# Kernel tuning notes

Hardware: AMD Instinct MI355X
Metric: run time of the kernel (lower is better)

## Reference

```python
import jax, jax.numpy as jnp
import numpy as np


def setup_inputs() -> dict:
    key = jax.random.key(0)
    ks = jax.random.split(key, 6)
    N, T, D, H = 256, 128, 512, 512
    x = jax.random.normal(ks[0], (N, T, D), dtype=jnp.float32)
    A = jax.random.normal(ks[1], (N, H, 4, 4), dtype=jnp.float32)
    Wx = jax.random.normal(ks[2], (D, 4 * H), dtype=jnp.float32) / np.sqrt(D)
    Wh = jax.random.normal(ks[3], (H, 4 * H), dtype=jnp.float32) / np.sqrt(H)
    Wattn = jax.random.normal(ks[4], (H, 4 * H), dtype=jnp.float32) / np.sqrt(H)
    b = jnp.zeros((4 * H,), dtype=jnp.float32)
    return {"x": x, "A": A, "Wx": Wx, "Wh": Wh, "Wattn": Wattn, "b": b}


def reference(x, A, Wx, Wh, Wattn, b):
    N, T, D = x.shape
    H = Wh.shape[0]
    A_flat = A.reshape(N, H, -1)  # (N, H, 16)
    h0 = A_flat.mean(axis=-1)     # mean over 4x4 grid
    c0 = h0
    inv_sqrt_H = 1.0 / np.sqrt(H).astype(np.float32)

    def step(carry, x_t):
        h, c = carry
        # scaled dot-product attention over the 16 spatial cells
        scores = jnp.einsum('nh,nhp->np', h, A_flat) * inv_sqrt_H  # (N, 16)
        w = jax.nn.softmax(scores, axis=-1)
        attn = jnp.einsum('nhp,np->nh', A_flat, w)                 # (N, H)
        a = x_t @ Wx + h @ Wh + attn @ Wattn + b                   # (N, 4H)
        a_i, a_f, a_o, a_g = jnp.split(a, 4, axis=1)
        i = jax.nn.sigmoid(a_i)
        f = jax.nn.sigmoid(a_f)
        o = jax.nn.sigmoid(a_o)
        g = jnp.tanh(a_g)
        c_next = f * c + i * g
        h_next = o * jnp.tanh(c_next)
        return (h_next, c_next), h_next

    _, hs = jax.lax.scan(step, (h0, c0), jnp.swapaxes(x, 0, 1))  # (T, N, H)
    return jnp.swapaxes(hs, 0, 1)  # (N, T, H)
```

## Files before the change

### kernel.cpp

```cpp
#include <hip/hip_runtime.h>
#include <math.h>

typedef unsigned short u16;
typedef _Float16 h16;
typedef _Float16 f16x8 __attribute__((ext_vector_type(8)));
typedef float f32x4 __attribute__((ext_vector_type(4)));

__device__ __forceinline__ float sigm(float x) { return 1.f / (1.f + expf(-x)); }


__global__ void k_pack_w(const float* __restrict__ Wx, const float* __restrict__ Wh,
                         h16* __restrict__ WhiS, h16* __restrict__ WloS) {
  unsigned idx = blockIdx.x * 256 + threadIdx.x;
  unsigned e = idx & 7, l = (idx >> 3) & 63, cf = (idx >> 9) & 1;
  unsigned t2 = idx >> 10;
  unsigned j = t2 >> 5, ks = t2 & 31;
  unsigned k = ks * 32 + ((l >> 4) << 3) + e;
  unsigned c32 = cf * 16 + (l & 15);
  unsigned acol = (c32 >> 3) * 512 + j * 8 + (c32 & 7);
  float v = (k < 512) ? Wx[(size_t)k * 2048 + acol]
                      : Wh[(size_t)(k - 512) * 2048 + acol];
  h16 hi = (h16)v;
  WhiS[idx] = hi;
  WloS[idx] = (h16)((v - (float)hi) * 4096.f);
}

__global__ __launch_bounds__(256) void k_m(const float* __restrict__ Af,
                                           const float* __restrict__ Wat,
                                           float* __restrict__ M2) {
  __shared__ float Alds[8192];
  const int tid = threadIdx.x;
  const int ct = blockIdx.x;
  const int n  = blockIdx.y;
  {
    const float4* src = (const float4*)(Af + (size_t)n * 8192);
    float4* dst = (float4*)Alds;
    for (int i = tid; i < 2048; i += 256) dst[i] = src[i];
  }
  __syncthreads();
  const int l = tid & 63, w = tid >> 6;
  const int col = ct * 64 + w * 16 + (l & 15);
  const int lq = l >> 4;
  f32x4 acc1 = {0.f, 0.f, 0.f, 0.f}, acc2 = {0.f, 0.f, 0.f, 0.f};
  for (int k0 = 0; k0 < 512; k0 += 32) {
    float av[8], wv[8];
#pragma unroll
    for (int e = 0; e < 8; ++e) av[e] = Alds[(k0 + lq * 8 + e) * 16 + (l & 15)];
#pragma unroll
    for (int e = 0; e < 8; ++e) wv[e] = Wat[(size_t)(k0 + lq * 8 + e) * 2048 + col];
    f16x8 Ah, Al_, Bh, Bl;
#pragma unroll
    for (int e = 0; e < 8; ++e) {
      h16 ah = (h16)av[e]; Ah[e] = ah; Al_[e] = (h16)((av[e] - (float)ah) * 4096.f);
      h16 bh = (h16)wv[e]; Bh[e] = bh; Bl[e]  = (h16)((wv[e] - (float)bh) * 4096.f);
    }
    acc1 = __builtin_amdgcn_mfma_f32_16x16x32_f16(Ah, Bh, acc1, 0, 0, 0);
    acc2 = __builtin_amdgcn_mfma_f32_16x16x32_f16(Al_, Bh, acc2, 0, 0, 0);
    acc2 = __builtin_amdgcn_mfma_f32_16x16x32_f16(Ah, Bl, acc2, 0, 0, 0);
  }
  float4 o;
  o.x = acc1[0] + acc2[0] * (1.f / 4096.f);
  o.y = acc1[1] + acc2[1] * (1.f / 4096.f);
  o.z = acc1[2] + acc2[2] * (1.f / 4096.f);
  o.w = acc1[3] + acc2[3] * (1.f / 4096.f);
  *(float4*)(M2 + ((size_t)n * 2048 + col) * 16 + lq * 4) = o;
}

__global__ void k_xsplit(const float* __restrict__ x, h16* __restrict__ xfhi,
                         h16* __restrict__ xflo) {
  unsigned tg = blockIdx.x * 256 + threadIdx.x;
  unsigned l = tg & 63, rt = (tg >> 6) & 1, ksg = (tg >> 7) & 15;
  unsigned g = (tg >> 11) & 7, t = tg >> 14;
  int n = g * 32 + rt * 16 + (l & 15);
  int k0 = ksg * 32 + (l >> 4) * 8;
  const float* xp = x + ((size_t)n * 128 + t) * 512 + k0;
  f32x4 v0 = *(const f32x4*)xp, v1 = *(const f32x4*)(xp + 4);
  float vv[8] = {v0[0], v0[1], v0[2], v0[3], v1[0], v1[1], v1[2], v1[3]};
  union { h16 h[8]; uint4 u; } a, b;
#pragma unroll
  for (int e = 0; e < 8; ++e) {
    h16 hh = (h16)vv[e];
    a.h[e] = hh;
    b.h[e] = (h16)((vv[e] - (float)hh) * 4096.f);
  }
  *(uint4*)(xfhi + (size_t)tg * 8) = a.u;
  *(uint4*)(xflo + (size_t)tg * 8) = b.u;
}

__global__ __launch_bounds__(512) void k_init(const float* __restrict__ Af,
                                              h16* __restrict__ hfhi,
                                              h16* __restrict__ hflo,
                                              float* __restrict__ cst,
                                              float* __restrict__ sb0) {
  const int n = blockIdx.x, k = threadIdx.x;
  float Areg[16];
  const f32x4* A4 = (const f32x4*)(Af + (size_t)n * 8192 + k * 16);
#pragma unroll
  for (int q4 = 0; q4 < 4; ++q4) {
    f32x4 v = A4[q4];
#pragma unroll
    for (int e = 0; e < 4; ++e) Areg[q4 * 4 + e] = v[e];
  }
  float s = 0.f;
#pragma unroll
  for (int p = 0; p < 16; ++p) s += Areg[p];
  s *= 0.0625f;
  cst[n * 512 + k] = s;
  h16 hh = (h16)s;
  const int g = n >> 5;
  const int hoff = ((((g * 16 + (k >> 5)) * 2 + ((n >> 4) & 1)) * 64 +
                     ((n & 15) | (((k >> 3) & 3) << 4))) * 8) + (k & 7);
  hfhi[hoff] = hh;
  hflo[hoff] = (h16)((s - (float)hh) * 4096.f);
  float ps[16];
#pragma unroll
  for (int p = 0; p < 16; ++p) ps[p] = s * Areg[p];
#pragma unroll
  for (int m = 1; m <= 4; m <<= 1)
#pragma unroll
    for (int p = 0; p < 16; ++p) ps[p] += __shfl_xor(ps[p], m);
  if ((k & 7) == 0) {
    float* o = sb0 + ((size_t)n * 64 + (k >> 3)) * 16;
#pragma unroll
    for (int p = 0; p < 16; ++p) o[p] = ps[p];
  }
}

template<bool XPRE>
__global__ __launch_bounds__(512, 4) void k_step(
    const float* __restrict__ bv, const float* __restrict__ Af,
    const float* __restrict__ x, const h16* __restrict__ xfhi, const h16* __restrict__ xflo,
    const h16* __restrict__ WhiS, const h16* __restrict__ WloS,
    const float* __restrict__ Mws,
    const float* __restrict__ sbR, float* __restrict__ sbW,
    h16* __restrict__ hfhi, h16* __restrict__ hflo,
    float* __restrict__ cst, float* __restrict__ out, int t) {
  __shared__ float P[7 * 1056];
  __shared__ float wsh[32][17];

  const int tid = threadIdx.x;
  const int l = tid & 63, wv = tid >> 6;
  const int bid = blockIdx.x;
  const int g = bid >> 6;
  const int j = (bid & 7) * 8 + ((bid >> 3) & 7);
  const int n0 = g * 32;

  {
    const int nS = tid >> 4, pS = tid & 15;
    const float* sr = sbR + ((size_t)(n0 + nS) * 64) * 16 + pS;
    float s = 0.f;
#pragma unroll 8
    for (int jj = 0; jj < 64; ++jj) s += sr[jj * 16];
    s *= 0.04419417382415922f;
    float m = s;
#pragma unroll
    for (int o = 8; o >= 1; o >>= 1) m = fmaxf(m, __shfl_xor(m, o, 16));
    float e = __expf(s - m);
    float se = e;
#pragma unroll
    for (int o = 8; o >= 1; o >>= 1) se += __shfl_xor(se, o, 16);
    wsh[nS][pS] = e / se;
  }

  const h16* whiJ = WhiS + (size_t)j * 32768;
  const h16* wloJ = WloS + (size_t)j * 32768;

  const int rC = tid >> 3, qC = tid & 7;
  const int colC = j * 8 + qC;
  const float b_i = bv[colC], b_f = bv[512 + colC], b_o = bv[1024 + colC],
              b_g = bv[1536 + colC];

  const int rb = t & 1, wb = rb ^ 1;
  const h16* hfhiR = hfhi + (size_t)rb * 131072;
  const h16* hfloR = hflo + (size_t)rb * 131072;

  f32x4 acc1[2][2], acc2[2][2];
#pragma unroll
  for (int rt = 0; rt < 2; ++rt)
#pragma unroll
    for (int cf = 0; cf < 2; ++cf) {
      acc1[rt][cf] = (f32x4){0.f, 0.f, 0.f, 0.f};
      acc2[rt][cf] = (f32x4){0.f, 0.f, 0.f, 0.f};
    }

  auto kstep = [&](int ksg) {
    const f16x8 bh0 = *(const f16x8*)(whiJ + ((size_t)(ksg * 2 + 0) * 64 + l) * 8);
    const f16x8 bh1 = *(const f16x8*)(whiJ + ((size_t)(ksg * 2 + 1) * 64 + l) * 8);
    const f16x8 bl0 = *(const f16x8*)(wloJ + ((size_t)(ksg * 2 + 0) * 64 + l) * 8);
    const f16x8 bl1 = *(const f16x8*)(wloJ + ((size_t)(ksg * 2 + 1) * 64 + l) * 8);
    f16x8 Ah[2], Al[2];
    if (ksg < 16) {
      if (XPRE) {
#pragma unroll
        for (int rt = 0; rt < 2; ++rt) {
          const size_t base = ((((size_t)t * 8 + g) * 16 + ksg) * 2 + rt) * 512 + l * 8;
          Ah[rt] = *(const f16x8*)(xfhi + base);
          Al[rt] = *(const f16x8*)(xflo + base);
        }
      } else {
#pragma unroll
        for (int rt = 0; rt < 2; ++rt) {
          const int n_x = g * 32 + rt * 16 + (l & 15);
          const int k_x = ksg * 32 + (l >> 4) * 8;
          const float* xp = x + ((size_t)n_x * 128 + t) * 512 + k_x;
          f32x4 v0 = *(const f32x4*)xp, v1 = *(const f32x4*)(xp + 4);
          float vv[8] = {v0[0], v0[1], v0[2], v0[3], v1[0], v1[1], v1[2], v1[3]};
#pragma unroll
          for (int e = 0; e < 8; ++e) {
            h16 hh = (h16)vv[e];
            Ah[rt][e] = hh;
            Al[rt][e] = (h16)((vv[e] - (float)hh) * 4096.f);
          }
        }
      }
    } else {
#pragma unroll
      for (int rt = 0; rt < 2; ++rt) {
        const size_t base = (((size_t)(g * 16 + (ksg - 16)) * 2 + rt) * 64 + l) * 8;
        Ah[rt] = *(const f16x8*)(hfhiR + base);
        Al[rt] = *(const f16x8*)(hfloR + base);
      }
    }
#pragma unroll
    for (int rt = 0; rt < 2; ++rt) {
      acc1[rt][0] = __builtin_amdgcn_mfma_f32_16x16x32_f16(Ah[rt], bh0, acc1[rt][0], 0, 0, 0);
      acc1[rt][1] = __builtin_amdgcn_mfma_f32_16x16x32_f16(Ah[rt], bh1, acc1[rt][1], 0, 0, 0);
      acc2[rt][0] = __builtin_amdgcn_mfma_f32_16x16x32_f16(Al[rt], bh0, acc2[rt][0], 0, 0, 0);
      acc2[rt][1] = __builtin_amdgcn_mfma_f32_16x16x32_f16(Al[rt], bh1, acc2[rt][1], 0, 0, 0);
      acc2[rt][0] = __builtin_amdgcn_mfma_f32_16x16x32_f16(Ah[rt], bl0, acc2[rt][0], 0, 0, 0);
      acc2[rt][1] = __builtin_amdgcn_mfma_f32_16x16x32_f16(Ah[rt], bl1, acc2[rt][1], 0, 0, 0);
    }
  };

#pragma unroll
  for (int i = 0; i < 4; ++i) kstep(wv + 8 * i);

  float accf[2][2][4];
#pragma unroll
  for (int rt = 0; rt < 2; ++rt)
#pragma unroll
    for (int cf = 0; cf < 2; ++cf)
#pragma unroll
      for (int rg = 0; rg < 4; ++rg)
        accf[rt][cf][rg] = acc1[rt][cf][rg] + acc2[rt][cf][rg] * (1.f / 4096.f);

  auto publish = [&](int slot) {
#pragma unroll
    for (int rt = 0; rt < 2; ++rt)
#pragma unroll
      for (int cf = 0; cf < 2; ++cf)
#pragma unroll
        for (int rg = 0; rg < 4; ++rg)
          P[slot * 1056 + (rt * 16 + (l >> 4) * 4 + rg) * 33 + cf * 16 + (l & 15)] =
              accf[rt][cf][rg];
  };
  auto addin = [&](int slot) {
#pragma unroll
    for (int rt = 0; rt < 2; ++rt)
#pragma unroll
      for (int cf = 0; cf < 2; ++cf)
#pragma unroll
        for (int rg = 0; rg < 4; ++rg)
          accf[rt][cf][rg] +=
              P[slot * 1056 + (rt * 16 + (l >> 4) * 4 + rg) * 33 + cf * 16 + (l & 15)];
  };

  if (wv >= 4) publish(wv - 4);
  __syncthreads();
  if (wv < 4) addin(wv);
  if (wv == 2) publish(4);
  if (wv == 3) publish(5);
  __syncthreads();
  if (wv == 0) addin(4);
  if (wv == 1) { addin(5); publish(6); }
  __syncthreads();
  if (wv == 0) { addin(6); publish(0); }
  __syncthreads();

  if (tid < 256) {
    const float* Mr = Mws + ((size_t)(n0 + rC) * 2048 + colC) * 16;
    float am[4];
#pragma unroll
    for (int f = 0; f < 4; ++f) {
      const float* mp = Mr + (size_t)f * 8192;
      float s = 0.f;
#pragma unroll
      for (int p = 0; p < 16; ++p) s += wsh[rC][p] * mp[p];
      am[f] = s;
    }
    float ai = P[rC * 33 + qC] + am[0] + b_i;
    float af_ = P[rC * 33 + 8 + qC] + am[1] + b_f;
    float ao = P[rC * 33 + 16 + qC] + am[2] + b_o;
    float ag = P[rC * 33 + 24 + qC] + am[3] + b_g;
    float ig = sigm(ai), fg = sigm(af_), og = sigm(ao), gg = tanhf(ag);
    const size_t cix = (size_t)(n0 + rC) * 512 + colC;
    float c = cst[cix];
    float cn = fg * c + ig * gg;
    cst[cix] = cn;
    float hn = og * tanhf(cn);
    h16 hh = (h16)hn;
    const int hoff = ((((g * 16 + (j >> 2)) * 2 + (rC >> 4)) * 64 +
                       ((rC & 15) | ((j & 3) << 4))) * 8) + qC;
    hfhi[(size_t)wb * 131072 + hoff] = hh;
    hflo[(size_t)wb * 131072 + hoff] = (h16)((hn - (float)hh) * 4096.f);
    out[((size_t)(n0 + rC) * 128 + t) * 512 + colC] = hn;

    float Areg[16];
    const f32x4* A4 = (const f32x4*)(Af + ((size_t)(n0 + rC) * 512 + colC) * 16);
#pragma unroll
    for (int q4 = 0; q4 < 4; ++q4) {
      f32x4 v = A4[q4];
#pragma unroll
      for (int e = 0; e < 4; ++e) Areg[q4 * 4 + e] = v[e];
    }
    float ps[16];
#pragma unroll
    for (int p = 0; p < 16; ++p) ps[p] = hn * Areg[p];
#pragma unroll
    for (int m = 1; m <= 4; m <<= 1)
#pragma unroll
      for (int p = 0; p < 16; ++p) ps[p] += __shfl_xor(ps[p], m);
    if (qC == 0) {
      float* o = sbW + ((size_t)(n0 + rC) * 64 + j) * 16;
#pragma unroll
      for (int p = 0; p < 16; ++p) o[p] = ps[p];
    }
  }
}


extern "C" void kernel_launch(void* const* d_in, const int* in_sizes, int n_in,
                              void* d_out, int out_size, void* d_ws, size_t ws_size,
                              hipStream_t stream) {
  (void)in_sizes; (void)n_in; (void)out_size;
  const float* x   = (const float*)d_in[0];
  const float* Af  = (const float*)d_in[1];
  const float* Wx  = (const float*)d_in[2];
  const float* Wh  = (const float*)d_in[3];
  const float* Wat = (const float*)d_in[4];
  const float* bv  = (const float*)d_in[5];
  float* out = (float*)d_out;

  char* ws = (char*)d_ws;
  size_t off = 0;
  auto alloc = [&](size_t nb) {
    char* p = ws + off; off = (off + nb + 255) & ~(size_t)255; return p;
  };
  h16*   WhiS = (h16*)alloc(2097152ull * 2);
  h16*   WloS = (h16*)alloc(2097152ull * 2);
  float* Mws  = (float*)alloc(8388608ull * 4);
  float* sb   = (float*)alloc(2ull * 262144 * 4);
  h16*   hfhi = (h16*)alloc(262144ull * 2);
  h16*   hflo = (h16*)alloc(262144ull * 2);
  float* cst  = (float*)alloc(131072ull * 4);
  size_t base_end = off;
  h16* xfhi = (h16*)alloc(16777216ull * 2);
  h16* xflo = (h16*)alloc(16777216ull * 2);
  bool xpre = (ws_size >= base_end + 2ull * 16777216ull * 2 + 4096);

  k_pack_w<<<8192, 256, 0, stream>>>(Wx, Wh, WhiS, WloS);
  k_m<<<dim3(32, 256), 256, 0, stream>>>(Af, Wat, Mws);
  k_init<<<256, 512, 0, stream>>>(Af, hfhi, hflo, cst, sb);
  if (xpre) k_xsplit<<<8192, 256, 0, stream>>>(x, xfhi, xflo);

  for (int t = 0; t < 128; ++t) {
    const float* sbR = sb + (size_t)(t & 1) * 262144;
    float* sbW = (float*)sb + (size_t)((t + 1) & 1) * 262144;
    if (xpre)
      k_step<true><<<512, 512, 0, stream>>>(bv, Af, x, xfhi, xflo, WhiS, WloS, Mws,
                                            sbR, sbW, hfhi, hflo, cst, out, t);
    else
      k_step<false><<<512, 512, 0, stream>>>(bv, Af, x, xfhi, xflo, WhiS, WloS, Mws,
                                             sbR, sbW, hfhi, hflo, cst, out, t);
  }
}
```

Before: 2.261 ms.

## Double batch rows per step block and prepack fp16 splits for attention GEMM

The recurrent step kernel now handles 64 batch rows per block instead of 32, halving the grid to 256 blocks. Each fetched Wx/Wh fp16 hi/lo weight fragment now feeds twice as many MFMAs, cutting weight reloads per step, and all 512 threads run the gate epilogue. Launch bounds drop to 2 waves per SIMD to leave room for the larger accumulator set. The one-time Af·Wattn precompute now reads inputs already split into fp16 hi/lo MFMA layouts by two new pack kernels, and each block computes 8 batch tiles so weight fragments are reused. The packed buffers alias the x-split workspace before k_xsplit overwrites it, which would go out of bounds if the workspace were too small.

```diff
diff --git a/kernel.cpp b/kernel.cpp
--- a/kernel.cpp
+++ b/kernel.cpp
@@ -25,45 +25,68 @@
   WloS[idx] = (h16)((v - (float)hi) * 4096.f);
 }
 
-__global__ __launch_bounds__(256) void k_m(const float* __restrict__ Af,
-                                           const float* __restrict__ Wat,
+__global__ void k_af_pack(const float* __restrict__ Af, h16* __restrict__ afhi,
+                          h16* __restrict__ aflo) {
+  unsigned idx = blockIdx.x * 256 + threadIdx.x;
+  unsigned e = idx & 7, l = (idx >> 3) & 63, ksg = (idx >> 9) & 15, n = idx >> 13;
+  unsigned k = ksg * 32 + ((l >> 4) << 3) + e;
+  float v = Af[(size_t)n * 8192 + k * 16 + (l & 15)];
+  h16 hi = (h16)v;
+  afhi[idx] = hi;
+  aflo[idx] = (h16)((v - (float)hi) * 4096.f);
+}
+
+__global__ void k_wat_pack(const float* __restrict__ Wat, h16* __restrict__ wathi,
+                           h16* __restrict__ watlo) {
+  unsigned idx = blockIdx.x * 256 + threadIdx.x;
+  unsigned e = idx & 7, l = (idx >> 3) & 63, ksg = (idx >> 9) & 15, cg = idx >> 13;
+  unsigned k = ksg * 32 + ((l >> 4) << 3) + e;
+  float v = Wat[(size_t)k * 2048 + cg * 16 + (l & 15)];
+  h16 hi = (h16)v;
+  wathi[idx] = hi;
+  watlo[idx] = (h16)((v - (float)hi) * 4096.f);
+}
+
+__global__ __launch_bounds__(256) void k_m(const h16* __restrict__ afhi,
+                                           const h16* __restrict__ aflo,
+                                           const h16* __restrict__ wathi,
+                                           const h16* __restrict__ watlo,
                                            float* __restrict__ M2) {
-  __shared__ float Alds[8192];
   const int tid = threadIdx.x;
-  const int ct = blockIdx.x;
-  const int n  = blockIdx.y;
-  {
-    const float4* src = (const float4*)(Af + (size_t)n * 8192);
-    float4* dst = (float4*)Alds;
-    for (int i = tid; i < 2048; i += 256) dst[i] = src[i];
-  }
-  __syncthreads();
+  const int ct = blockIdx.x, ng = blockIdx.y;
   const int l = tid & 63, w = tid >> 6;
-  const int col = ct * 64 + w * 16 + (l & 15);
+  const int cg = ct * 4 + w;
+  const int col = cg * 16 + (l & 15);
   const int lq = l >> 4;
-  f32x4 acc1 = {0.f, 0.f, 0.f, 0.f}, acc2 = {0.f, 0.f, 0.f, 0.f};
-  for (int k0 = 0; k0 < 512; k0 += 32) {
-    float av[8], wv[8];
-#pragma unroll
-    for (int e = 0; e < 8; ++e) av[e] = Alds[(k0 + lq * 8 + e) * 16 + (l & 15)];
-#pragma unroll
-    for (int e = 0; e < 8; ++e) wv[e] = Wat[(size_t)(k0 + lq * 8 + e) * 2048 + col];
-    f16x8 Ah, Al_, Bh, Bl;
-#pragma unroll
-    for (int e = 0; e < 8; ++e) {
-      h16 ah = (h16)av[e]; Ah[e] = ah; Al_[e] = (h16)((av[e] - (float)ah) * 4096.f);
-      h16 bh = (h16)wv[e]; Bh[e] = bh; Bl[e]  = (h16)((wv[e] - (float)bh) * 4096.f);
-    }
-    acc1 = __builtin_amdgcn_mfma_f32_16x16x32_f16(Ah, Bh, acc1, 0, 0, 0);
-    acc2 = __builtin_amdgcn_mfma_f32_16x16x32_f16(Al_, Bh, acc2, 0, 0, 0);
-    acc2 = __builtin_amdgcn_mfma_f32_16x16x32_f16(Ah, Bl, acc2, 0, 0, 0);
-  }
-  float4 o;
-  o.x = acc1[0] + acc2[0] * (1.f / 4096.f);
-  o.y = acc1[1] + acc2[1] * (1.f / 4096.f);
-  o.z = acc1[2] + acc2[2] * (1.f / 4096.f);
-  o.w = acc1[3] + acc2[3] * (1.f / 4096.f);
-  *(float4*)(M2 + ((size_t)n * 2048 + col) * 16 + lq * 4) = o;
+  f32x4 acc1[8], acc2[8];
+#pragma unroll
+  for (int i = 0; i < 8; ++i) {
+    acc1[i] = (f32x4){0.f, 0.f, 0.f, 0.f};
+    acc2[i] = (f32x4){0.f, 0.f, 0.f, 0.f};
+  }
+  for (int ksg = 0; ksg < 16; ++ksg) {
+    const size_t boff = (((size_t)cg * 16 + ksg) * 64 + l) * 8;
+    const f16x8 bh = *(const f16x8*)(wathi + boff);
+    const f16x8 bl = *(const f16x8*)(watlo + boff);
+#pragma unroll
+    for (int i = 0; i < 8; ++i) {
+      const size_t aoff = (((size_t)(ng * 8 + i) * 16 + ksg) * 64 + l) * 8;
+      const f16x8 ah = *(const f16x8*)(afhi + aoff);
+      const f16x8 al = *(const f16x8*)(aflo + aoff);
+      acc1[i] = __builtin_amdgcn_mfma_f32_16x16x32_f16(ah, bh, acc1[i], 0, 0, 0);
+      acc2[i] = __builtin_amdgcn_mfma_f32_16x16x32_f16(al, bh, acc2[i], 0, 0, 0);
+      acc2[i] = __builtin_amdgcn_mfma_f32_16x16x32_f16(ah, bl, acc2[i], 0, 0, 0);
+    }
+  }
+#pragma unroll
+  for (int i = 0; i < 8; ++i) {
+    float4 o;
+    o.x = acc1[i][0] + acc2[i][0] * (1.f / 4096.f);
+    o.y = acc1[i][1] + acc2[i][1] * (1.f / 4096.f);
+    o.z = acc1[i][2] + acc2[i][2] * (1.f / 4096.f);
+    o.w = acc1[i][3] + acc2[i][3] * (1.f / 4096.f);
+    *(float4*)(M2 + ((size_t)(ng * 8 + i) * 2048 + col) * 16 + lq * 4) = o;
+  }
 }
 
 __global__ void k_xsplit(const float* __restrict__ x, h16* __restrict__ xfhi,
@@ -127,7 +150,7 @@
 }
 
 template<bool XPRE>
-__global__ __launch_bounds__(512, 4) void k_step(
+__global__ __launch_bounds__(512, 2) void k_step(
     const float* __restrict__ bv, const float* __restrict__ Af,
     const float* __restrict__ x, const h16* __restrict__ xfhi, const h16* __restrict__ xflo,
     const h16* __restrict__ WhiS, const h16* __restrict__ WloS,
@@ -135,18 +158,19 @@
     const float* __restrict__ sbR, float* __restrict__ sbW,
     h16* __restrict__ hfhi, h16* __restrict__ hflo,
     float* __restrict__ cst, float* __restrict__ out, int t) {
-  __shared__ float P[7 * 1056];
-  __shared__ float wsh[32][17];
+  __shared__ float P[7 * 2112];
+  __shared__ float wsh[64][17];
 
   const int tid = threadIdx.x;
   const int l = tid & 63, wv = tid >> 6;
   const int bid = blockIdx.x;
-  const int g = bid >> 6;
+  const int gp = bid >> 6;
   const int j = (bid & 7) * 8 + ((bid >> 3) & 7);
-  const int n0 = g * 32;
-
-  {
-    const int nS = tid >> 4, pS = tid & 15;
+  const int n0 = gp * 64;
+
+#pragma unroll
+  for (int half = 0; half < 2; ++half) {
+    const int nS = (tid >> 4) + half * 32, pS = tid & 15;
     const float* sr = sbR + ((size_t)(n0 + nS) * 64) * 16 + pS;
     float s = 0.f;
 #pragma unroll 8
@@ -174,9 +198,9 @@
   const h16* hfhiR = hfhi + (size_t)rb * 131072;
   const h16* hfloR = hflo + (size_t)rb * 131072;
 
-  f32x4 acc1[2][2], acc2[2][2];
-#pragma unroll
-  for (int rt = 0; rt < 2; ++rt)
+  f32x4 acc1[4][2], acc2[4][2];
+#pragma unroll
+  for (int rt = 0; rt < 4; ++rt)
 #pragma unroll
     for (int cf = 0; cf < 2; ++cf) {
       acc1[rt][cf] = (f32x4){0.f, 0.f, 0.f, 0.f};
@@ -188,19 +212,20 @@
     const f16x8 bh1 = *(const f16x8*)(whiJ + ((size_t)(ksg * 2 + 1) * 64 + l) * 8);
     const f16x8 bl0 = *(const f16x8*)(wloJ + ((size_t)(ksg * 2 + 0) * 64 + l) * 8);
     const f16x8 bl1 = *(const f16x8*)(wloJ + ((size_t)(ksg * 2 + 1) * 64 + l) * 8);
-    f16x8 Ah[2], Al[2];
+    f16x8 Ah[4], Al[4];
     if (ksg < 16) {
       if (XPRE) {
 #pragma unroll
-        for (int rt = 0; rt < 2; ++rt) {
-          const size_t base = ((((size_t)t * 8 + g) * 16 + ksg) * 2 + rt) * 512 + l * 8;
+        for (int rt = 0; rt < 4; ++rt) {
+          const int og = gp * 2 + (rt >> 1), ort = rt & 1;
+          const size_t base = ((((size_t)t * 8 + og) * 16 + ksg) * 2 + ort) * 512 + l * 8;
           Ah[rt] = *(const f16x8*)(xfhi + base);
           Al[rt] = *(const f16x8*)(xflo + base);
         }
       } else {
 #pragma unroll
-        for (int rt = 0; rt < 2; ++rt) {
-          const int n_x = g * 32 + rt * 16 + (l & 15);
+        for (int rt = 0; rt < 4; ++rt) {
+          const int n_x = n0 + rt * 16 + (l & 15);
           const int k_x = ksg * 32 + (l >> 4) * 8;
           const float* xp = x + ((size_t)n_x * 128 + t) * 512 + k_x;
           f32x4 v0 = *(const f32x4*)xp, v1 = *(const f32x4*)(xp + 4);
@@ -215,14 +240,15 @@
       }
     } else {
 #pragma unroll
-      for (int rt = 0; rt < 2; ++rt) {
-        const size_t base = (((size_t)(g * 16 + (ksg - 16)) * 2 + rt) * 64 + l) * 8;
+      for (int rt = 0; rt < 4; ++rt) {
+        const int og = gp * 2 + (rt >> 1), ort = rt & 1;
+        const size_t base = (((size_t)(og * 16 + (ksg - 16)) * 2 + ort) * 64 + l) * 8;
         Ah[rt] = *(const f16x8*)(hfhiR + base);
         Al[rt] = *(const f16x8*)(hfloR + base);
       }
     }
 #pragma unroll
-    for (int rt = 0; rt < 2; ++rt) {
+    for (int rt = 0; rt < 4; ++rt) {
       acc1[rt][0] = __builtin_amdgcn_mfma_f32_16x16x32_f16(Ah[rt], bh0, acc1[rt][0], 0, 0, 0);
       acc1[rt][1] = __builtin_amdgcn_mfma_f32_16x16x32_f16(Ah[rt], bh1, acc1[rt][1], 0, 0, 0);
       acc2[rt][0] = __builtin_amdgcn_mfma_f32_16x16x32_f16(Al[rt], bh0, acc2[rt][0], 0, 0, 0);
@@ -235,9 +261,9 @@
 #pragma unroll
   for (int i = 0; i < 4; ++i) kstep(wv + 8 * i);
 
-  float accf[2][2][4];
-#pragma unroll
-  for (int rt = 0; rt < 2; ++rt)
+  float accf[4][2][4];
+#pragma unroll
+  for (int rt = 0; rt < 4; ++rt)
 #pragma unroll
     for (int cf = 0; cf < 2; ++cf)
 #pragma unroll
@@ -246,23 +272,23 @@
 
   auto publish = [&](int slot) {
 #pragma unroll
-    for (int rt = 0; rt < 2; ++rt)
+    for (int rt = 0; rt < 4; ++rt)
 #pragma unroll
       for (int cf = 0; cf < 2; ++cf)
 #pragma unroll
         for (int rg = 0; rg < 4; ++rg)
-          P[slot * 1056 + (rt * 16 + (l >> 4) * 4 + rg) * 33 + cf * 16 + (l & 15)] =
+          P[slot * 2112 + (rt * 16 + (l >> 4) * 4 + rg) * 33 + cf * 16 + (l & 15)] =
               accf[rt][cf][rg];
   };
   auto addin = [&](int slot) {
 #pragma unroll
-    for (int rt = 0; rt < 2; ++rt)
+    for (int rt = 0; rt < 4; ++rt)
 #pragma unroll
       for (int cf = 0; cf < 2; ++cf)
 #pragma unroll
         for (int rg = 0; rg < 4; ++rg)
           accf[rt][cf][rg] +=
-              P[slot * 1056 + (rt * 16 + (l >> 4) * 4 + rg) * 33 + cf * 16 + (l & 15)];
+              P[slot * 2112 + (rt * 16 + (l >> 4) * 4 + rg) * 33 + cf * 16 + (l & 15)];
   };
 
   if (wv >= 4) publish(wv - 4);
@@ -277,7 +303,7 @@
   if (wv == 0) { addin(6); publish(0); }
   __syncthreads();
 
-  if (tid < 256) {
+  {
     const float* Mr = Mws + ((size_t)(n0 + rC) * 2048 + colC) * 16;
     float am[4];
 #pragma unroll
@@ -292,21 +318,22 @@
     float af_ = P[rC * 33 + 8 + qC] + am[1] + b_f;
     float ao = P[rC * 33 + 16 + qC] + am[2] + b_o;
     float ag = P[rC * 33 + 24 + qC] + am[3] + b_g;
-    float ig = sigm(ai), fg = sigm(af_), og = sigm(ao), gg = tanhf(ag);
-    const size_t cix = (size_t)(n0 + rC) * 512 + colC;
+    float ig = sigm(ai), fg = sigm(af_), og_ = sigm(ao), gg = tanhf(ag);
+    const int n = n0 + rC;
+    const size_t cix = (size_t)n * 512 + colC;
     float c = cst[cix];
     float cn = fg * c + ig * gg;
     cst[cix] = cn;
-    float hn = og * tanhf(cn);
+    float hn = og_ * tanhf(cn);
     h16 hh = (h16)hn;
-    const int hoff = ((((g * 16 + (j >> 2)) * 2 + (rC >> 4)) * 64 +
-                       ((rC & 15) | ((j & 3) << 4))) * 8) + qC;
+    const int hoff = (((((n >> 5) * 16 + (j >> 2)) * 2 + ((n >> 4) & 1)) * 64 +
+                       ((n & 15) | ((j & 3) << 4))) * 8) + qC;
     hfhi[(size_t)wb * 131072 + hoff] = hh;
     hflo[(size_t)wb * 131072 + hoff] = (h16)((hn - (float)hh) * 4096.f);
-    out[((size_t)(n0 + rC) * 128 + t) * 512 + colC] = hn;
+    out[((size_t)n * 128 + t) * 512 + colC] = hn;
 
     float Areg[16];
-    const f32x4* A4 = (const f32x4*)(Af + ((size_t)(n0 + rC) * 512 + colC) * 16);
+    const f32x4* A4 = (const f32x4*)(Af + ((size_t)n * 512 + colC) * 16);
 #pragma unroll
     for (int q4 = 0; q4 < 4; ++q4) {
       f32x4 v = A4[q4];
@@ -321,7 +348,7 @@
 #pragma unroll
       for (int p = 0; p < 16; ++p) ps[p] += __shfl_xor(ps[p], m);
     if (qC == 0) {
-      float* o = sbW + ((size_t)(n0 + rC) * 64 + j) * 16;
+      float* o = sbW + ((size_t)n * 64 + j) * 16;
 #pragma unroll
       for (int p = 0; p < 16; ++p) o[p] = ps[p];
     }
@@ -358,8 +385,15 @@
   h16* xflo = (h16*)alloc(16777216ull * 2);
   bool xpre = (ws_size >= base_end + 2ull * 16777216ull * 2 + 4096);
 
+  h16* afhi  = xfhi;
+  h16* aflo  = xfhi + 2097152;
+  h16* wathi = xfhi + 2ull * 2097152;
+  h16* watlo = xfhi + 3ull * 2097152;
+
   k_pack_w<<<8192, 256, 0, stream>>>(Wx, Wh, WhiS, WloS);
-  k_m<<<dim3(32, 256), 256, 0, stream>>>(Af, Wat, Mws);
+  k_af_pack<<<8192, 256, 0, stream>>>(Af, afhi, aflo);
+  k_wat_pack<<<4096, 256, 0, stream>>>(Wat, wathi, watlo);
+  k_m<<<dim3(32, 32), 256, 0, stream>>>(afhi, aflo, wathi, watlo, Mws);
   k_init<<<256, 512, 0, stream>>>(Af, hfhi, hflo, cst, sb);
   if (xpre) k_xsplit<<<8192, 256, 0, stream>>>(x, xfhi, xflo);
 
@@ -367,10 +401,10 @@
     const float* sbR = sb + (size_t)(t & 1) * 262144;
     float* sbW = (float*)sb + (size_t)((t + 1) & 1) * 262144;
     if (xpre)
-      k_step<true><<<512, 512, 0, stream>>>(bv, Af, x, xfhi, xflo, WhiS, WloS, Mws,
+      k_step<true><<<256, 512, 0, stream>>>(bv, Af, x, xfhi, xflo, WhiS, WloS, Mws,
                                             sbR, sbW, hfhi, hflo, cst, out, t);
     else
-      k_step<false><<<512, 512, 0, stream>>>(bv, Af, x, xfhi, xflo, WhiS, WloS, Mws,
+      k_step<false><<<256, 512, 0, stream>>>(bv, Af, x, xfhi, xflo, WhiS, WloS, Mws,
                                              sbR, sbW, hfhi, hflo, cst, out, t);
   }
 }
```

Result: slower. 2.668 ms (+18.0%).
